# Optimization experiments

Measured on AMD Instinct MI355X. Metric: run time of the kernel, lower is better.

The kernel has to match this reference:

```python
import jax, jax.numpy as jnp
import numpy as np

N = 20000      # atoms
E = 240000     # edges (avg degree ~12, matches _AVG_DEGREE_MATPES)
C = 128        # sphere_channels
ZMAX = 100     # max_num_elements
NG = 600       # GaussianSmearing(0, cutoff, 600, 2.0)
CUTOFF = 6.0
WIDTH = 2.0    # basis_width_scalar
RESCALE = 12.0 # _AVG_DEGREE_MATPES
LN_EPS = 1e-5
# xyz -> (y,z,x): real-SH component order for l=1, so Wigner D^(1) = P R P^T
P = np.array([[0.,1.,0.],[0.,0.,1.],[1.,0.,0.]], dtype=np.float32)


def _layernorm(x, g, b):
    mu = jnp.mean(x, axis=-1, keepdims=True)
    var = jnp.mean((x - mu) ** 2, axis=-1, keepdims=True)
    return g * (x - mu) * jax.lax.rsqrt(var + LN_EPS) + b


def init_edge_rot_mat(ev):
    # faithful port of init_edge_rot_mat (torch uses .detach())
    ev = jax.lax.stop_gradient(ev)
    dist = jnp.maximum(jnp.linalg.norm(ev, axis=1, keepdims=True), 1e-8)
    nx = ev / dist
    ref = jnp.eye(3, dtype=ev.dtype)[jnp.argmin(jnp.abs(nx), axis=1)]
    nz = jnp.cross(nx, ref)
    nz = nz / jnp.maximum(jnp.linalg.norm(nz, axis=1, keepdims=True), 1e-8)
    ny = jnp.cross(nx, nz)
    ny = ny / jnp.maximum(jnp.linalg.norm(ny, axis=1, keepdims=True), 1e-8)
    # edge_rot_mat_inv has columns [nz, nx, -ny]; rot = inv^T -> rows [nz, nx, -ny]
    return jnp.stack([nz, nx, -ny], axis=1)  # [E,3,3]


def setup_inputs() -> dict:
    key = jax.random.key(0)
    ks = jax.random.split(key, 10)
    s = 0.02
    return {
        'edge_distance_vec': jax.random.normal(ks[0], (E, 3), jnp.float32) * 2.0,
        'sphere_emb': jax.random.normal(ks[1], (ZMAX, C), jnp.float32) * s,
        'src_emb': jax.random.normal(ks[2], (ZMAX, C), jnp.float32) * s,
        'tgt_emb': jax.random.normal(ks[3], (ZMAX, C), jnp.float32) * s,
        'W1': jax.random.normal(ks[4], (NG + 2 * C, C), jnp.float32) * s,
        'b1': jnp.zeros((C,), jnp.float32),
        'g1': jnp.ones((C,), jnp.float32),
        'be1': jnp.zeros((C,), jnp.float32),
        'W2': jax.random.normal(ks[5], (C, C), jnp.float32) * s,
        'b2': jnp.zeros((C,), jnp.float32),
        'g2': jnp.ones((C,), jnp.float32),
        'be2': jnp.zeros((C,), jnp.float32),
        'W3': jax.random.normal(ks[6], (C, 2 * C), jnp.float32) * s,
        'b3': jnp.zeros((2 * C,), jnp.float32),
        'atomic_numbers': jax.random.randint(ks[7], (N,), 0, ZMAX),
        'edge_index': jax.random.randint(ks[8], (2, E), 0, N),
    }


def reference(edge_distance_vec, sphere_emb, src_emb, tgt_emb,
              W1, b1, g1, be1, W2, b2, g2, be2, W3, b3,
              atomic_numbers, edge_index):
    src, dst = edge_index[0], edge_index[1]
    Pm = jnp.asarray(P)
    # per-edge rotation to edge-aligned frame and its l=1 Wigner matrix
    rot = init_edge_rot_mat(edge_distance_vec)               # [E,3,3]
    D1 = jnp.einsum('ij,ejk,lk->eil', Pm, rot, Pm)           # [E,3,3]
    # Gaussian distance expansion (600 basis fns)
    dist = jnp.linalg.norm(edge_distance_vec, axis=1)        # [E]
    offsets = jnp.linspace(0.0, CUTOFF, NG)
    coeff = -0.5 / (WIDTH * (offsets[1] - offsets[0])) ** 2
    gauss = jnp.exp(coeff * (dist[:, None] - offsets[None, :]) ** 2)  # [E,600]
    # edge features: distance basis + source/target atom embeddings
    x_edge = jnp.concatenate(
        [gauss, src_emb[atomic_numbers[src]], tgt_emb[atomic_numbers[dst]]], axis=1)
    # RadialFunction: Linear->LN->SiLU x2, final Linear -> m=0 coefficients
    h = jax.nn.silu(_layernorm(x_edge @ W1 + b1, g1, be1))
    h = jax.nn.silu(_layernorm(h @ W2 + b2, g2, be2))
    m0 = (h @ W3 + b3).reshape(E, 2, C)   # (l=0,m=0) and (l=1,m=0)
    # rotate back to global frame: blockdiag(1, D1)^T applied to (m0[0]; 0, m0[1], 0)
    l0 = m0[:, 0][:, None, :]                                 # [E,1,C]
    l1 = jnp.einsum('ei,ec->eic', D1[:, 1, :], m0[:, 1])      # (D1^T v)_i with v=(0,a,0)
    msg = jnp.concatenate([l0, l1], axis=1)                   # [E,4,C]
    # scatter-sum messages to target nodes, rescale by avg degree
    x_deg = jnp.zeros((N, 4, C), msg.dtype).at[dst].add(msg) / RESCALE
    # node init: atom embedding into l=0 slot, plus edge-degree embedding
    x = x_deg.at[:, 0].add(sphere_emb[atomic_numbers])
    return x
```

## Files before the change

### kernel.cpp

```cpp
#include <hip/hip_runtime.h>
#include <stdint.h>

#define EE 240000
#define NN 20000
#define NB 4096

typedef __attribute__((ext_vector_type(4))) float f32x4;
typedef __attribute__((ext_vector_type(8))) __bf16 bf16x8;
typedef __attribute__((ext_vector_type(8))) short s16x8;

union V8 { s16x8 s; bf16x8 b; };

static constexpr float GC2 =
    (float)((-0.5 / ((12.0 / 599.0) * (12.0 / 599.0))) * 1.4426950408889634);

__device__ __forceinline__ float b2f(unsigned short u) {
    return __uint_as_float(((unsigned)u) << 16);
}
__device__ __forceinline__ unsigned short f2b(float f) {
    unsigned u = __float_as_uint(f);
    return (unsigned short)((u + 0x7fffu + ((u >> 16) & 1u)) >> 16);
}
__device__ __forceinline__ unsigned short ldc(const void* p, int i, bool isb) {
    return isb ? ((const unsigned short*)p)[i] : f2b(((const float*)p)[i]);
}
__device__ __forceinline__ float ldf(const void* p, int i, bool isb) {
    return isb ? b2f(((const unsigned short*)p)[i]) : ((const float*)p)[i];
}
__device__ __forceinline__ bool probe_isb(const void* g1) {
    return ((const unsigned*)g1)[0] != 0x3F800000u;
}

#define PREP_PARAMS_TOTAL (114688 + 16384 + 32768 + 2 * 12800 + 6 * 128 + 256)
#define PB ((PREP_PARAMS_TOTAL + 255) / 256)
#define EB ((EE + 255) / 256)

__global__ void prep_all(const void* ev, const int* __restrict__ an,
                         const int* __restrict__ ei,
                         const void* W1, const void* W2, const void* W3,
                         const void* se, const void* te,
                         const void* b1, const void* g1, const void* be1,
                         const void* b2, const void* g2, const void* be2,
                         const void* b3,
                         unsigned short* __restrict__ W1T,
                         unsigned short* __restrict__ W2T,
                         unsigned short* __restrict__ W3T,
                         unsigned short* __restrict__ SE,
                         unsigned short* __restrict__ TE,
                         unsigned short* __restrict__ vecs,
                         uint4* __restrict__ sedge_u, float4* __restrict__ d1_out,
                         int* __restrict__ deg, int* __restrict__ bhist) {
    bool isb = probe_isb(g1);
    int bid = blockIdx.x;
    if (bid < PB) {
        int t = bid * 256 + threadIdx.x;
        if (t < 114688) {
            int j = t & 7, n = (t >> 3) & 127, kb = t >> 10;
            int k = kb * 8 + j;
            unsigned short v = 0;
            if (k < 600) v = ldc(W1, k * 128 + n, isb);
            else if (k >= 608 && k < 864) v = ldc(W1, (k - 8) * 128 + n, isb);
            W1T[t] = v;
            return;
        }
        t -= 114688;
        if (t < 16384) {
            int j = t & 7, n = (t >> 3) & 127, kb = t >> 10;
            W2T[t] = ldc(W2, (kb * 8 + j) * 128 + n, isb);
            return;
        }
        t -= 16384;
        if (t < 32768) {
            int j = t & 7, n = (t >> 3) & 255, kb = t >> 11;
            W3T[t] = ldc(W3, (kb * 8 + j) * 256 + n, isb);
            return;
        }
        t -= 32768;
        if (t < 12800) { SE[t] = ldc(se, t, isb); return; }
        t -= 12800;
        if (t < 12800) { TE[t] = ldc(te, t, isb); return; }
        t -= 12800;
        if (t < 128) { vecs[t] = ldc(b1, t, isb); return; }
        t -= 128;
        if (t < 128) { vecs[128 + t] = ldc(g1, t, isb); return; }
        t -= 128;
        if (t < 128) { vecs[256 + t] = ldc(be1, t, isb); return; }
        t -= 128;
        if (t < 128) { vecs[384 + t] = ldc(b2, t, isb); return; }
        t -= 128;
        if (t < 128) { vecs[512 + t] = ldc(g2, t, isb); return; }
        t -= 128;
        if (t < 128) { vecs[640 + t] = ldc(be2, t, isb); return; }
        t -= 128;
        if (t < 256) { vecs[768 + t] = ldc(b3, t, isb); return; }
        return;
    }
    int e = (bid - PB) * 256 + threadIdx.x;
    if (e >= EE) return;
    float x = ldf(ev, e * 3 + 0, isb);
    float y = ldf(ev, e * 3 + 1, isb);
    float z = ldf(ev, e * 3 + 2, isb);
    float nrm = sqrtf(x * x + y * y + z * z);
    float dc = fmaxf(nrm, 1e-8f);
    float nx0 = x / dc, nx1 = y / dc, nx2 = z / dc;
    float a0 = fabsf(nx0), a1 = fabsf(nx1), a2 = fabsf(nx2);
    int idx = 0; float mv = a0;
    if (a1 < mv) { idx = 1; mv = a1; }
    if (a2 < mv) { idx = 2; }
    float r0 = (idx == 0) ? 1.f : 0.f;
    float r1 = (idx == 1) ? 1.f : 0.f;
    float r2 = (idx == 2) ? 1.f : 0.f;
    float z0 = nx1 * r2 - nx2 * r1;
    float z1 = nx2 * r0 - nx0 * r2;
    float z2 = nx0 * r1 - nx1 * r0;
    float zn = fmaxf(sqrtf(z0 * z0 + z1 * z1 + z2 * z2), 1e-8f);
    z0 /= zn; z1 /= zn; z2 /= zn;
    float y0 = nx1 * z2 - nx2 * z1;
    float y1 = nx2 * z0 - nx0 * z2;
    float y2 = nx0 * z1 - nx1 * z0;
    float yn = fmaxf(sqrtf(y0 * y0 + y1 * y1 + y2 * y2), 1e-8f);
    y0 /= yn; y1 /= yn; y2 /= yn;
    float4 dv; dv.x = -y1; dv.y = -y2; dv.z = -y0; dv.w = 0.f;
    d1_out[e] = dv;
    int zsv = an[ei[e]];
    int dst = ei[EE + e];
    int zdv = an[dst];
    uint4 su;
    su.x = __float_as_uint(nrm);
    su.y = (unsigned)zsv | ((unsigned)zdv << 16);
    su.z = (unsigned)e;
    su.w = 0;
    sedge_u[e] = su;
    atomicAdd(&deg[dst], 1);
    int b = min(NB - 1, (int)(nrm * 512.0f));
    atomicAdd(&bhist[b], 1);
}

__global__ __launch_bounds__(1024) void scan_all(
    const int* __restrict__ deg, const int* __restrict__ bhist,
    int* __restrict__ row_start, int* __restrict__ cursor, int* __restrict__ bcursor) {
    __shared__ int lds[1024];
    int t = threadIdx.x;
    int base = t * 20;
    int loc[20]; int ls = 0;
#pragma unroll
    for (int j = 0; j < 20; ++j) {
        int i = base + j;
        ls += (i < NN) ? deg[i] : 0;
        loc[j] = ls;
    }
    lds[t] = ls; __syncthreads();
    for (int s = 1; s < 1024; s <<= 1) {
        int v = (t >= s) ? lds[t - s] : 0;
        __syncthreads(); lds[t] += v; __syncthreads();
    }
    int off = lds[t] - ls;
#pragma unroll
    for (int j = 0; j < 20; ++j) {
        int i = base + j;
        if (i < NN) {
            row_start[i + 1] = off + loc[j];
            cursor[i] = off + (j ? loc[j - 1] : 0);
        }
    }
    if (t == 0) row_start[0] = 0;
    __syncthreads();
    int b4 = t * 4;
    int l4[4]; int bs = 0;
#pragma unroll
    for (int j = 0; j < 4; ++j) { bs += bhist[b4 + j]; l4[j] = bs; }
    lds[t] = bs; __syncthreads();
    for (int s = 1; s < 1024; s <<= 1) {
        int v = (t >= s) ? lds[t - s] : 0;
        __syncthreads(); lds[t] += v; __syncthreads();
    }
    int boff = lds[t] - bs;
#pragma unroll
    for (int j = 0; j < 4; ++j) bcursor[b4 + j] = boff + (j ? l4[j - 1] : 0);
}

__global__ void fill_sorted(const int* __restrict__ ei,
                            const uint4* __restrict__ sedge_u,
                            const float4* __restrict__ d1v,
                            int* __restrict__ cursor, int* __restrict__ bcursor,
                            uint4* __restrict__ sedge_s, float4* __restrict__ d1s) {
    int e = blockIdx.x * 256 + threadIdx.x;
    if (e >= EE) return;
    uint4 su = sedge_u[e];
    int dst = ei[EE + e];
    int p = atomicAdd(&cursor[dst], 1);
    float d = __uint_as_float(su.x);
    int b = min(NB - 1, (int)(d * 512.0f));
    int sp = atomicAdd(&bcursor[b], 1);
    su.z = (unsigned)p;
    sedge_s[sp] = su;
    d1s[p] = d1v[e];
}

__device__ __forceinline__ void ln_silu(f32x4 (&acc)[8],
                                        const unsigned short* __restrict__ bias,
                                        const unsigned short* __restrict__ gamma,
                                        const unsigned short* __restrict__ beta,
                                        int i16, int quad,
                                        unsigned short (*ht)[136]) {
    float bb[8];
#pragma unroll
    for (int nt = 0; nt < 8; ++nt) bb[nt] = b2f(bias[nt * 16 + i16]);
#pragma unroll
    for (int r = 0; r < 4; ++r) {
        float v[8]; float s = 0.f, s2 = 0.f;
#pragma unroll
        for (int nt = 0; nt < 8; ++nt) {
            v[nt] = acc[nt][r] + bb[nt];
            s += v[nt]; s2 += v[nt] * v[nt];
        }
#pragma unroll
        for (int m = 1; m < 16; m <<= 1) {
            s += __shfl_xor(s, m);
            s2 += __shfl_xor(s2, m);
        }
        float mu = s * (1.f / 128.f);
        float var = s2 * (1.f / 128.f) - mu * mu;
        float rs = rsqrtf(var + 1e-5f);
        int row = quad * 4 + r;
#pragma unroll
        for (int nt = 0; nt < 8; ++nt) {
            int c = nt * 16 + i16;
            float y = b2f(gamma[c]) * (v[nt] - mu) * rs + b2f(beta[c]);
            float sg = __builtin_amdgcn_rcpf(1.f + exp2f(-1.4426950409f * y));
            ht[row][c] = f2b(y * sg);
        }
    }
}

template <bool MSG>
__global__ __launch_bounds__(256, 6) void edge_mlp(
    const unsigned short* __restrict__ W1T, const unsigned short* __restrict__ W2T,
    const unsigned short* __restrict__ W3T,
    const unsigned short* __restrict__ SE, const unsigned short* __restrict__ TE,
    const unsigned short* __restrict__ vecs,
    const uint4* __restrict__ sedge,
    const int* __restrict__ ei, const float4* __restrict__ d1v,
    unsigned short* __restrict__ msg0, unsigned short* __restrict__ msg1,
    float* __restrict__ xacc) {
    __shared__ __align__(16) unsigned short htile_s[4][16][136];
    int tid = threadIdx.x;
    int wave = tid >> 6, lane = tid & 63;
    int i16 = lane & 15, quad = lane >> 4;
    unsigned short (*ht)[136] = htile_s[wave];
    int mbase = blockIdx.x * 64 + wave * 16;

    uint4 s0 = sedge[mbase + i16];
    float dd = __uint_as_float(s0.x);
    int seo = (int)(s0.y & 0xFFFFu) * 128;
    int teo = (int)(s0.y >> 16) * 128;
    int dpz = (int)s0.z;

    float dmn = dd, dmx = dd;
#pragma unroll
    for (int m = 1; m < 64; m <<= 1) {
        dmn = fminf(dmn, __shfl_xor(dmn, m));
        dmx = fmaxf(dmx, __shfl_xor(dmx, m));
    }
    int klo = (int)floorf((dmn - 0.285f) * (599.0f / 6.0f));
    int khi = (int)ceilf((dmx + 0.285f) * (599.0f / 6.0f));
    int ka = min(max(klo, 0) >> 5, 19);
    int kb = min((min(khi, 607) >> 5) + 1, 19);

    f32x4 acc[8];
#pragma unroll
    for (int nt = 0; nt < 8; ++nt)
#pragma unroll
        for (int q = 0; q < 4; ++q) acc[nt][q] = 0.f;

#pragma unroll 1
    for (int ks = ka; ks < kb; ++ks) {
        int k0 = ks * 32 + quad * 8;
        V8 af;
#pragma unroll
        for (int j = 0; j < 8; ++j) {
            float t = dd - (float)(k0 + j) * (6.0f / 599.0f);
            af.s[j] = (short)f2b(exp2f(GC2 * t * t));
        }
        const unsigned short* w1p = W1T + (((ks * 4 + quad) * 128 + i16) << 3);
#pragma unroll
        for (int nt = 0; nt < 8; ++nt) {
            V8 bf_; bf_.s = *(const s16x8*)(w1p + nt * 128);
            acc[nt] = __builtin_amdgcn_mfma_f32_16x16x32_bf16(af.b, bf_.b, acc[nt], 0, 0, 0);
        }
    }
#pragma unroll 1
    for (int ks = 19; ks < 27; ++ks) {
        int k0 = ks * 32 + quad * 8;
        V8 af;
        if (ks < 23) af.s = *(const s16x8*)(SE + seo + (k0 - 608));
        else         af.s = *(const s16x8*)(TE + teo + (k0 - 736));
        const unsigned short* w1p = W1T + (((ks * 4 + quad) * 128 + i16) << 3);
#pragma unroll
        for (int nt = 0; nt < 8; ++nt) {
            V8 bf_; bf_.s = *(const s16x8*)(w1p + nt * 128);
            acc[nt] = __builtin_amdgcn_mfma_f32_16x16x32_bf16(af.b, bf_.b, acc[nt], 0, 0, 0);
        }
    }
    ln_silu(acc, vecs + 0, vecs + 128, vecs + 256, i16, quad, ht);

#pragma unroll
    for (int nt = 0; nt < 8; ++nt)
#pragma unroll
        for (int q = 0; q < 4; ++q) acc[nt][q] = 0.f;
#pragma unroll 1
    for (int ks = 0; ks < 4; ++ks) {
        int k0 = ks * 32 + quad * 8;
        V8 a0;
        a0.s = *(const s16x8*)&ht[i16][k0];
        const unsigned short* w2p = W2T + (((ks * 4 + quad) * 128 + i16) << 3);
#pragma unroll
        for (int nt = 0; nt < 8; ++nt) {
            V8 bf_; bf_.s = *(const s16x8*)(w2p + nt * 128);
            acc[nt] = __builtin_amdgcn_mfma_f32_16x16x32_bf16(a0.b, bf_.b, acc[nt], 0, 0, 0);
        }
    }
    ln_silu(acc, vecs + 384, vecs + 512, vecs + 640, i16, quad, ht);

#pragma unroll 1
    for (int half = 0; half < 2; ++half) {
#pragma unroll
        for (int nt = 0; nt < 8; ++nt)
#pragma unroll
            for (int q = 0; q < 4; ++q) acc[nt][q] = 0.f;
#pragma unroll 1
        for (int ks = 0; ks < 4; ++ks) {
            int k0 = ks * 32 + quad * 8;
            V8 a0;
            a0.s = *(const s16x8*)&ht[i16][k0];
            const unsigned short* w3p = W3T + (((ks * 4 + quad) * 256 + half * 128 + i16) << 3);
#pragma unroll
            for (int nt = 0; nt < 8; ++nt) {
                V8 bf_; bf_.s = *(const s16x8*)(w3p + nt * 128);
                acc[nt] = __builtin_amdgcn_mfma_f32_16x16x32_bf16(a0.b, bf_.b, acc[nt], 0, 0, 0);
            }
        }
        if constexpr (MSG) {
            unsigned short* marr = half == 0 ? msg0 : msg1;
            float bo[8];
#pragma unroll
            for (int nt = 0; nt < 8; ++nt)
                bo[nt] = b2f(vecs[768 + half * 128 + nt * 16 + i16]);
#pragma unroll
            for (int r = 0; r < 4; ++r) {
                int dp = __shfl(dpz, quad * 4 + r);
                unsigned short* mrow = marr + (size_t)dp * 128 + i16;
#pragma unroll
                for (int nt = 0; nt < 8; ++nt)
                    mrow[nt * 16] = f2b(acc[nt][r] + bo[nt]);
            }
        } else {
#pragma unroll
            for (int r = 0; r < 4; ++r) {
                int eidx = mbase + quad * 4 + r;
                int dn = ei[EE + eidx];
                float* xb = xacc + (size_t)dn * 512;
                if (half == 0) {
#pragma unroll
                    for (int nt = 0; nt < 8; ++nt)
                        atomicAdd(xb + nt * 16 + i16,
                                  acc[nt][r] + b2f(vecs[768 + nt * 16 + i16]));
                } else {
                    float4 dv = d1v[eidx];
#pragma unroll
                    for (int nt = 0; nt < 8; ++nt) {
                        float val = acc[nt][r] + b2f(vecs[896 + nt * 16 + i16]);
                        atomicAdd(xb + 128 + nt * 16 + i16, val * dv.x);
                        atomicAdd(xb + 256 + nt * 16 + i16, val * dv.y);
                        atomicAdd(xb + 384 + nt * 16 + i16, val * dv.z);
                    }
                }
            }
        }
    }
}

__global__ __launch_bounds__(256) void gather(
    const unsigned short* __restrict__ msg0, const unsigned short* __restrict__ msg1,
    const float4* __restrict__ d1s, const int* __restrict__ row_start,
    const void* __restrict__ sp, const void* __restrict__ g1,
    const int* __restrict__ an, float* __restrict__ out) {
    int tid = threadIdx.x;
    int n = blockIdx.x * 4 + (tid >> 6);
    int c = (tid & 63) * 2;
    bool isb = probe_isb(g1);
    int i0 = row_start[n], i1 = row_start[n + 1];
    float s0a = 0.f, s0b = 0.f, sxa = 0.f, sxb = 0.f,
          sya = 0.f, syb = 0.f, sza = 0.f, szb = 0.f;
#pragma unroll 2
    for (int i = i0; i < i1; ++i) {
        unsigned m0 = *(const unsigned*)(msg0 + (size_t)i * 128 + c);
        unsigned m1 = *(const unsigned*)(msg1 + (size_t)i * 128 + c);
        float4 dv = d1s[i];
        float o0a = b2f((unsigned short)m0), o0b = b2f((unsigned short)(m0 >> 16));
        float o1a = b2f((unsigned short)m1), o1b = b2f((unsigned short)(m1 >> 16));
        s0a += o0a; s0b += o0b;
        sxa += o1a * dv.x; sxb += o1b * dv.x;
        sya += o1a * dv.y; syb += o1b * dv.y;
        sza += o1a * dv.z; szb += o1b * dv.z;
    }
    float* ob = out + (size_t)n * 512;
    int zb = an[n] * 128 + c;
    float2 w;
    w.x = s0a * (1.f / 12.f) + ldf(sp, zb, isb);
    w.y = s0b * (1.f / 12.f) + ldf(sp, zb + 1, isb);
    *(float2*)(ob + c) = w;
    w.x = sxa * (1.f / 12.f); w.y = sxb * (1.f / 12.f);
    *(float2*)(ob + 128 + c) = w;
    w.x = sya * (1.f / 12.f); w.y = syb * (1.f / 12.f);
    *(float2*)(ob + 256 + c) = w;
    w.x = sza * (1.f / 12.f); w.y = szb * (1.f / 12.f);
    *(float2*)(ob + 384 + c) = w;
}

__global__ void finalize(const float* __restrict__ xacc, const void* __restrict__ sp,
                         const void* __restrict__ g1,
                         const int* __restrict__ an, float* __restrict__ out) {
    int t = blockIdx.x * 256 + threadIdx.x;
    bool isb = probe_isb(g1);
    int n = t >> 9, sc = t & 511;
    float v = xacc[t] * (1.f / 12.f);
    if (sc < 128) v += ldf(sp, an[n] * 128 + sc, isb);
    out[t] = v;
}

extern "C" void kernel_launch(void* const* d_in, const int* in_sizes, int n_in,
                              void* d_out, int out_size, void* d_ws, size_t ws_size,
                              hipStream_t stream) {
    const void* ev         = d_in[0];
    const void* sphere_emb = d_in[1];
    const void* src_emb    = d_in[2];
    const void* tgt_emb    = d_in[3];
    const void* W1  = d_in[4];  const void* b1  = d_in[5];
    const void* g1  = d_in[6];  const void* be1 = d_in[7];
    const void* W2  = d_in[8];  const void* b2  = d_in[9];
    const void* g2  = d_in[10]; const void* be2 = d_in[11];
    const void* W3  = d_in[12]; const void* b3  = d_in[13];
    const int* an   = (const int*)d_in[14];
    const int* ei   = (const int*)d_in[15];

    char* ws = (char*)d_ws;
    const size_t NEED_MSG = 132000000;

    if (ws_size >= NEED_MSG) {
        size_t off = 0;
        unsigned short* msg0 = (unsigned short*)(ws + off); off += (size_t)EE * 128 * 2;
        unsigned short* msg1 = (unsigned short*)(ws + off); off += (size_t)EE * 128 * 2;
        uint4* sedge_u = (uint4*)(ws + 0);
        float4* d1v    = (float4*)(ws + 3840000);
        float4* d1s    = (float4*)(ws + off);  off += (size_t)EE * 16;
        uint4* sedge_s = (uint4*)(ws + off);   off += (size_t)EE * 16;
        int* deg       = (int*)(ws + off);     off += (size_t)NN * 4;
        int* bhist     = (int*)(ws + off);     off += NB * 4;
        int* row_start = (int*)(ws + off);     off += (size_t)(NN + 4) * 4;
        int* cursor    = (int*)(ws + off);     off += (size_t)NN * 4;
        int* bcursor   = (int*)(ws + off);     off += NB * 4;
        unsigned short* W1T = (unsigned short*)(ws + off); off += 128 * 896 * 2;
        unsigned short* W2T = (unsigned short*)(ws + off); off += 128 * 128 * 2;
        unsigned short* W3T = (unsigned short*)(ws + off); off += 256 * 128 * 2;
        unsigned short* SEc = (unsigned short*)(ws + off); off += 100 * 128 * 2;
        unsigned short* TEc = (unsigned short*)(ws + off); off += 100 * 128 * 2;
        unsigned short* vecs = (unsigned short*)(ws + off); off += 1024 * 2;

        hipMemsetAsync(deg, 0, (size_t)(NN + NB) * 4, stream);
        prep_all<<<PB + EB, 256, 0, stream>>>(
            ev, an, ei, W1, W2, W3, src_emb, tgt_emb,
            b1, g1, be1, b2, g2, be2, b3,
            W1T, W2T, W3T, SEc, TEc, vecs, sedge_u, d1v, deg, bhist);
        scan_all<<<1, 1024, 0, stream>>>(deg, bhist, row_start, cursor, bcursor);
        fill_sorted<<<(EE + 255) / 256, 256, 0, stream>>>(
            ei, sedge_u, d1v, cursor, bcursor, sedge_s, d1s);
        edge_mlp<true><<<EE / 64, 256, 0, stream>>>(
            W1T, W2T, W3T, SEc, TEc, vecs, sedge_s,
            (const int*)nullptr, (const float4*)nullptr, msg0, msg1, (float*)nullptr);
        gather<<<NN / 4, 256, 0, stream>>>(msg0, msg1, d1s, row_start,
                                           sphere_emb, g1, an, (float*)d_out);
    } else {
        size_t off = 0;
        float* xacc    = (float*)(ws + off);   off += (size_t)NN * 512 * 4;
        uint4* sedge_u = (uint4*)(ws + off);   off += (size_t)EE * 16;
        float4* d1v    = (float4*)(ws + off);  off += (size_t)EE * 16;
        int* deg       = (int*)(ws + off);     off += (size_t)NN * 4;
        int* bhist     = (int*)(ws + off);     off += NB * 4;
        unsigned short* W1T = (unsigned short*)(ws + off); off += 128 * 896 * 2;
        unsigned short* W2T = (unsigned short*)(ws + off); off += 128 * 128 * 2;
        unsigned short* W3T = (unsigned short*)(ws + off); off += 256 * 128 * 2;
        unsigned short* SEc = (unsigned short*)(ws + off); off += 100 * 128 * 2;
        unsigned short* TEc = (unsigned short*)(ws + off); off += 100 * 128 * 2;
        unsigned short* vecs = (unsigned short*)(ws + off); off += 1024 * 2;

        hipMemsetAsync(xacc, 0, (size_t)NN * 512 * 4, stream);
        hipMemsetAsync(deg, 0, (size_t)(NN + NB) * 4, stream);
        prep_all<<<PB + EB, 256, 0, stream>>>(
            ev, an, ei, W1, W2, W3, src_emb, tgt_emb,
            b1, g1, be1, b2, g2, be2, b3,
            W1T, W2T, W3T, SEc, TEc, vecs, sedge_u, d1v, deg, bhist);
        edge_mlp<false><<<EE / 64, 256, 0, stream>>>(
            W1T, W2T, W3T, SEc, TEc, vecs, sedge_u, ei, d1v,
            (unsigned short*)nullptr, (unsigned short*)nullptr, xacc);
        finalize<<<(NN * 512) / 256, 256, 0, stream>>>(xacc, sphere_emb, g1, an,
                                                       (float*)d_out);
    }
}
```

Measured before the change: 352.4 us.

## Interleave message layout and use packed bf16 conversion with permuted weight rows

Replaces the software round-to-nearest bf16 conversion with the hardware v_cvt_pk_bf16_f32 instruction, which packs two floats per instruction for Gaussian features, hidden activations and messages. Channels are stored as interleaved pairs (nt, nt+1) so each lane writes 32-bit words, and the W2/W3 rows are permuted to match the new hidden-tile column order. The two message arrays merge into one 512-byte row per edge, and gather is rewritten so half the wave handles l=0 and half handles l=1 with wider loads. The aim is fewer conversion ALU ops and fewer, wider memory transactions, at the cost of more complex index mapping in gather and a layout-dependent weight permutation.

```diff
diff --git a/kernel.cpp b/kernel.cpp
--- a/kernel.cpp
+++ b/kernel.cpp
@@ -9,7 +9,7 @@
 typedef __attribute__((ext_vector_type(8))) __bf16 bf16x8;
 typedef __attribute__((ext_vector_type(8))) short s16x8;
 
-union V8 { s16x8 s; bf16x8 b; };
+union V8 { s16x8 s; bf16x8 b; uint4 u; };
 
 static constexpr float GC2 =
     (float)((-0.5 / ((12.0 / 599.0) * (12.0 / 599.0))) * 1.4426950408889634);
@@ -21,6 +21,11 @@
     unsigned u = __float_as_uint(f);
     return (unsigned short)((u + 0x7fffu + ((u >> 16) & 1u)) >> 16);
 }
+__device__ __forceinline__ unsigned cvtpk(float lo, float hi) {
+    unsigned r;
+    asm("v_cvt_pk_bf16_f32 %0, %1, %2" : "=v"(r) : "v"(lo), "v"(hi));
+    return r;
+}
 __device__ __forceinline__ unsigned short ldc(const void* p, int i, bool isb) {
     return isb ? ((const unsigned short*)p)[i] : f2b(((const float*)p)[i]);
 }
@@ -29,6 +34,11 @@
 }
 __device__ __forceinline__ bool probe_isb(const void* g1) {
     return ((const unsigned*)g1)[0] != 0x3F800000u;
+}
+
+__device__ __forceinline__ int kperm(int p) {
+    int wi = p >> 1;
+    return ((wi >> 4) << 5) + (wi & 15) + ((p & 1) << 4);
 }
 
 #define PREP_PARAMS_TOTAL (114688 + 16384 + 32768 + 2 * 12800 + 6 * 128 + 256)
@@ -66,13 +76,13 @@
         t -= 114688;
         if (t < 16384) {
             int j = t & 7, n = (t >> 3) & 127, kb = t >> 10;
-            W2T[t] = ldc(W2, (kb * 8 + j) * 128 + n, isb);
+            W2T[t] = ldc(W2, kperm(kb * 8 + j) * 128 + n, isb);
             return;
         }
         t -= 16384;
         if (t < 32768) {
             int j = t & 7, n = (t >> 3) & 255, kb = t >> 11;
-            W3T[t] = ldc(W3, (kb * 8 + j) * 256 + n, isb);
+            W3T[t] = ldc(W3, kperm(kb * 8 + j) * 256 + n, isb);
             return;
         }
         t -= 32768;
@@ -222,13 +232,17 @@
         float mu = s * (1.f / 128.f);
         float var = s2 * (1.f / 128.f) - mu * mu;
         float rs = rsqrtf(var + 1e-5f);
-        int row = quad * 4 + r;
-#pragma unroll
-        for (int nt = 0; nt < 8; ++nt) {
-            int c = nt * 16 + i16;
-            float y = b2f(gamma[c]) * (v[nt] - mu) * rs + b2f(beta[c]);
-            float sg = __builtin_amdgcn_rcpf(1.f + exp2f(-1.4426950409f * y));
-            ht[row][c] = f2b(y * sg);
+        unsigned* wrow = (unsigned*)ht[quad * 4 + r];
+#pragma unroll
+        for (int ntp = 0; ntp < 4; ++ntp) {
+            float zz[2];
+#pragma unroll
+            for (int h = 0; h < 2; ++h) {
+                int c = (2 * ntp + h) * 16 + i16;
+                float y = b2f(gamma[c]) * (v[2 * ntp + h] - mu) * rs + b2f(beta[c]);
+                zz[h] = y * __builtin_amdgcn_rcpf(1.f + exp2f(-1.4426950409f * y));
+            }
+            wrow[ntp * 16 + i16] = cvtpk(zz[0], zz[1]);
         }
     }
 }
@@ -241,8 +255,7 @@
     const unsigned short* __restrict__ vecs,
     const uint4* __restrict__ sedge,
     const int* __restrict__ ei, const float4* __restrict__ d1v,
-    unsigned short* __restrict__ msg0, unsigned short* __restrict__ msg1,
-    float* __restrict__ xacc) {
+    unsigned* __restrict__ msg, float* __restrict__ xacc) {
     __shared__ __align__(16) unsigned short htile_s[4][16][136];
     int tid = threadIdx.x;
     int wave = tid >> 6, lane = tid & 63;
@@ -276,12 +289,17 @@
 #pragma unroll 1
     for (int ks = ka; ks < kb; ++ks) {
         int k0 = ks * 32 + quad * 8;
-        V8 af;
+        float e[8];
 #pragma unroll
         for (int j = 0; j < 8; ++j) {
             float t = dd - (float)(k0 + j) * (6.0f / 599.0f);
-            af.s[j] = (short)f2b(exp2f(GC2 * t * t));
-        }
+            e[j] = exp2f(GC2 * t * t);
+        }
+        V8 af;
+        af.u.x = cvtpk(e[0], e[1]);
+        af.u.y = cvtpk(e[2], e[3]);
+        af.u.z = cvtpk(e[4], e[5]);
+        af.u.w = cvtpk(e[6], e[7]);
         const unsigned short* w1p = W1T + (((ks * 4 + quad) * 128 + i16) << 3);
 #pragma unroll
         for (int nt = 0; nt < 8; ++nt) {
@@ -341,7 +359,6 @@
             }
         }
         if constexpr (MSG) {
-            unsigned short* marr = half == 0 ? msg0 : msg1;
             float bo[8];
 #pragma unroll
             for (int nt = 0; nt < 8; ++nt)
@@ -349,10 +366,11 @@
 #pragma unroll
             for (int r = 0; r < 4; ++r) {
                 int dp = __shfl(dpz, quad * 4 + r);
-                unsigned short* mrow = marr + (size_t)dp * 128 + i16;
-#pragma unroll
-                for (int nt = 0; nt < 8; ++nt)
-                    mrow[nt * 16] = f2b(acc[nt][r] + bo[nt]);
+                unsigned* mrow = msg + (size_t)dp * 128 + half * 64 + i16;
+#pragma unroll
+                for (int ntp = 0; ntp < 4; ++ntp)
+                    mrow[ntp * 16] = cvtpk(acc[2 * ntp][r] + bo[2 * ntp],
+                                           acc[2 * ntp + 1][r] + bo[2 * ntp + 1]);
             }
         } else {
 #pragma unroll
@@ -381,41 +399,54 @@
 }
 
 __global__ __launch_bounds__(256) void gather(
-    const unsigned short* __restrict__ msg0, const unsigned short* __restrict__ msg1,
+    const unsigned* __restrict__ msg,
     const float4* __restrict__ d1s, const int* __restrict__ row_start,
     const void* __restrict__ sp, const void* __restrict__ g1,
     const int* __restrict__ an, float* __restrict__ out) {
     int tid = threadIdx.x;
     int n = blockIdx.x * 4 + (tid >> 6);
-    int c = (tid & 63) * 2;
+    int l = tid & 63;
+    int l2 = l & 31;
+    bool hi = l >= 32;
+    int c = ((l2 >> 3) << 5) | ((2 * l2) & 15);
     bool isb = probe_isb(g1);
     int i0 = row_start[n], i1 = row_start[n + 1];
-    float s0a = 0.f, s0b = 0.f, sxa = 0.f, sxb = 0.f,
-          sya = 0.f, syb = 0.f, sza = 0.f, szb = 0.f;
+    float s0 = 0.f, s1 = 0.f, s2 = 0.f, s3 = 0.f;
+    float yy0 = 0.f, yy1 = 0.f, yy2 = 0.f, yy3 = 0.f;
+    float zz0 = 0.f, zz1 = 0.f, zz2 = 0.f, zz3 = 0.f;
 #pragma unroll 2
     for (int i = i0; i < i1; ++i) {
-        unsigned m0 = *(const unsigned*)(msg0 + (size_t)i * 128 + c);
-        unsigned m1 = *(const unsigned*)(msg1 + (size_t)i * 128 + c);
-        float4 dv = d1s[i];
-        float o0a = b2f((unsigned short)m0), o0b = b2f((unsigned short)(m0 >> 16));
-        float o1a = b2f((unsigned short)m1), o1b = b2f((unsigned short)(m1 >> 16));
-        s0a += o0a; s0b += o0b;
-        sxa += o1a * dv.x; sxb += o1b * dv.x;
-        sya += o1a * dv.y; syb += o1b * dv.y;
-        sza += o1a * dv.z; szb += o1b * dv.z;
+        uint2 mv = *(const uint2*)(msg + (size_t)i * 128 + l * 2);
+        float v0 = b2f((unsigned short)mv.x), v1 = b2f((unsigned short)(mv.x >> 16));
+        float v2 = b2f((unsigned short)mv.y), v3 = b2f((unsigned short)(mv.y >> 16));
+        if (!hi) {
+            s0 += v0; s1 += v1; s2 += v2; s3 += v3;
+        } else {
+            float4 dv = d1s[i];
+            s0 += v0 * dv.x; s1 += v1 * dv.x; s2 += v2 * dv.x; s3 += v3 * dv.x;
+            yy0 += v0 * dv.y; yy1 += v1 * dv.y; yy2 += v2 * dv.y; yy3 += v3 * dv.y;
+            zz0 += v0 * dv.z; zz1 += v1 * dv.z; zz2 += v2 * dv.z; zz3 += v3 * dv.z;
+        }
     }
     float* ob = out + (size_t)n * 512;
-    int zb = an[n] * 128 + c;
+    constexpr float R = 1.f / 12.f;
     float2 w;
-    w.x = s0a * (1.f / 12.f) + ldf(sp, zb, isb);
-    w.y = s0b * (1.f / 12.f) + ldf(sp, zb + 1, isb);
-    *(float2*)(ob + c) = w;
-    w.x = sxa * (1.f / 12.f); w.y = sxb * (1.f / 12.f);
-    *(float2*)(ob + 128 + c) = w;
-    w.x = sya * (1.f / 12.f); w.y = syb * (1.f / 12.f);
-    *(float2*)(ob + 256 + c) = w;
-    w.x = sza * (1.f / 12.f); w.y = szb * (1.f / 12.f);
-    *(float2*)(ob + 384 + c) = w;
+    if (!hi) {
+        int zb = an[n] * 128 + c;
+        w.x = s0 * R + ldf(sp, zb, isb);
+        w.y = s2 * R + ldf(sp, zb + 1, isb);
+        *(float2*)(ob + c) = w;
+        w.x = s1 * R + ldf(sp, zb + 16, isb);
+        w.y = s3 * R + ldf(sp, zb + 17, isb);
+        *(float2*)(ob + c + 16) = w;
+    } else {
+        w.x = s0 * R;  w.y = s2 * R;  *(float2*)(ob + 128 + c) = w;
+        w.x = s1 * R;  w.y = s3 * R;  *(float2*)(ob + 128 + c + 16) = w;
+        w.x = yy0 * R; w.y = yy2 * R; *(float2*)(ob + 256 + c) = w;
+        w.x = yy1 * R; w.y = yy3 * R; *(float2*)(ob + 256 + c + 16) = w;
+        w.x = zz0 * R; w.y = zz2 * R; *(float2*)(ob + 384 + c) = w;
+        w.x = zz1 * R; w.y = zz3 * R; *(float2*)(ob + 384 + c + 16) = w;
+    }
 }
 
 __global__ void finalize(const float* __restrict__ xacc, const void* __restrict__ sp,
@@ -449,8 +480,7 @@
 
     if (ws_size >= NEED_MSG) {
         size_t off = 0;
-        unsigned short* msg0 = (unsigned short*)(ws + off); off += (size_t)EE * 128 * 2;
-        unsigned short* msg1 = (unsigned short*)(ws + off); off += (size_t)EE * 128 * 2;
+        unsigned* msg = (unsigned*)(ws + off); off += (size_t)EE * 512;
         uint4* sedge_u = (uint4*)(ws + 0);
         float4* d1v    = (float4*)(ws + 3840000);
         float4* d1s    = (float4*)(ws + off);  off += (size_t)EE * 16;
@@ -477,8 +507,8 @@
             ei, sedge_u, d1v, cursor, bcursor, sedge_s, d1s);
         edge_mlp<true><<<EE / 64, 256, 0, stream>>>(
             W1T, W2T, W3T, SEc, TEc, vecs, sedge_s,
-            (const int*)nullptr, (const float4*)nullptr, msg0, msg1, (float*)nullptr);
-        gather<<<NN / 4, 256, 0, stream>>>(msg0, msg1, d1s, row_start,
+            (const int*)nullptr, (const float4*)nullptr, msg, (float*)nullptr);
+        gather<<<NN / 4, 256, 0, stream>>>(msg, d1s, row_start,
                                            sphere_emb, g1, an, (float*)d_out);
     } else {
         size_t off = 0;
@@ -502,7 +532,7 @@
             W1T, W2T, W3T, SEc, TEc, vecs, sedge_u, d1v, deg, bhist);
         edge_mlp<false><<<EE / 64, 256, 0, stream>>>(
             W1T, W2T, W3T, SEc, TEc, vecs, sedge_u, ei, d1v,
-            (unsigned short*)nullptr, (unsigned short*)nullptr, xacc);
+            (unsigned*)nullptr, xacc);
         finalize<<<(NN * 512) / 256, 256, 0, stream>>>(xacc, sphere_emb, g1, an,
                                                        (float*)d_out);
     }
```

Result: slower. 362.7 us (+2.9%).
